# Kernel tuning notes

Measured on AMD Instinct MI355X. Metric: run time of the kernel, lower is better.

## Reference

```python
import jax, jax.numpy as jnp
import numpy as np

MIN_NORM = 1e-15
BALL_EPS = 4e-3  # fp32 boundary eps used by HGCN PoincareBall.proj
C = 1.0
RATIO = 0.75


def _norm(x):
    return jnp.clip(jnp.sqrt(jnp.sum(x * x, axis=-1, keepdims=True)), MIN_NORM)


def artanh(x):
    return jnp.arctanh(jnp.clip(x, -1.0 + 1e-7, 1.0 - 1e-7))


def proj(x, c):
    n = _norm(x)
    maxnorm = (1.0 - BALL_EPS) / jnp.sqrt(c)
    return jnp.where(n > maxnorm, x / n * maxnorm, x)


def expmap0(u, c):
    sc = jnp.sqrt(c)
    un = _norm(u)
    return jnp.tanh(sc * un) * u / (sc * un)


def logmap0(p, c):
    sc = jnp.sqrt(c)
    pn = _norm(p)
    return artanh(sc * pn) * p / (sc * pn)


def mobius_matvec(m, x, c):
    sc = jnp.sqrt(c)
    xn = _norm(x)
    mx = x @ m.T  # [N, out]
    mxn = _norm(mx)
    res = jnp.tanh(mxn / xn * artanh(sc * xn)) * mx / (mxn * sc)
    zero = jnp.all(mx == 0, axis=-1, keepdims=True)
    return jnp.where(zero, jnp.zeros_like(res), res)


def mobius_add(x, y, c):
    x2 = jnp.sum(x * x, axis=-1, keepdims=True)
    y2 = jnp.sum(y * y, axis=-1, keepdims=True)
    xy = jnp.sum(x * y, axis=-1, keepdims=True)
    num = (1 + 2 * c * xy + c * y2) * x + (1 - c * x2) * y
    den = 1 + 2 * c * xy + c * c * x2 * y2
    return num / jnp.maximum(den, MIN_NORM)


def hyp_linear(x, W, b, c):
    res = proj(mobius_matvec(W, x, c), c)
    hb = proj(expmap0(b[None, :], c), c)  # proj_tan0 is identity in Poincare ball
    return proj(mobius_add(res, hb, c), c)


def setup_inputs() -> dict:
    key = jax.random.key(0)
    k = jax.random.split(key, 6)
    N, E, D_IN, D_OUT = 50000, 800000, 128, 64
    x = 0.01 * jax.random.normal(k[0], (N, D_IN), jnp.float32)  # points near origin of ball
    W = jax.random.normal(k[1], (D_OUT, D_IN), jnp.float32) * np.sqrt(2.0 / (D_IN + D_OUT))
    b = 0.01 * jax.random.normal(k[2], (D_OUT,), jnp.float32)
    beta_W = jax.random.normal(k[3], (1, 2 * D_OUT), jnp.float32) * np.sqrt(2.0 / (2 * D_OUT + 1))
    beta_b = 0.01 * jax.random.normal(k[4], (1,), jnp.float32)
    edge_index = jax.random.randint(k[5], (2, E), 0, N, dtype=jnp.int64)
    return {"x": x, "W": W, "b": b, "beta_W": beta_W, "beta_b": beta_b, "edge_index": edge_index}


def reference(x, W, b, beta_W, beta_b, edge_index):
    N = x.shape[0]
    src, dst = edge_index[0], edge_index[1]  # PyG: x_j = x[src], aggregated at dst
    agg = lambda v: jax.ops.segment_sum(v[src], dst, num_segments=N)

    updated_x = hyp_linear(x, W, b, C)
    updated_tanx = logmap0(updated_x, C)

    # NodeInformationScore: (I - D^{-1/2} A D^{-1/2}) x, self loops removed (weight 0)
    w = jnp.where(src == dst, 0.0, 1.0).astype(x.dtype)
    deg = jax.ops.segment_sum(w, src, num_segments=N)
    dinv = jnp.where(deg > 0, deg ** -0.5, 0.0)
    norm_e = dinv[src] * w * dinv[dst]  # [E]
    neigh = jax.ops.segment_sum(norm_e[:, None] * updated_tanx[src], dst, num_segments=N)
    info = updated_tanx - neigh
    score = jnp.sum(jnp.abs(info), axis=1)  # [N]

    k = int(N * RATIO)
    T = jax.lax.top_k(score, k)[0][-1]  # min of top-k values
    sel = (score > T).astype(x.dtype)[:, None]  # [N, 1] hard gate

    sum_neigh = agg(updated_tanx)
    sum_sel = agg(sel * updated_tanx)
    concat = jnp.concatenate([sum_sel, sum_neigh], axis=-1)  # [N, 2*out]
    hyp_sums = proj(expmap0(concat, C), C)

    beta_out = hyp_linear(hyp_sums, beta_W, beta_b, C)  # [N, 1]
    w_sel = jax.nn.sigmoid(logmap0(beta_out, C))  # [N, 1]

    A_x = jax.nn.relu(agg(w_sel * sel * updated_tanx))
    out = proj(expmap0(updated_tanx + A_x, C), C)
    return out
```

## Files before the change

kernel.cpp:

```cpp
#include <hip/hip_runtime.h>
#include <math.h>
#include <limits.h>


__device__ __forceinline__ float wredsum(float v) {
#pragma unroll
    for (int off = 32; off > 0; off >>= 1) v += __shfl_xor(v, off, 64);
    return v;
}

__device__ __forceinline__ float rdlane_f(float v, int i) {
    return __uint_as_float(__builtin_amdgcn_readlane(__float_as_uint(v), i));
}

__device__ __forceinline__ int bitonic64(int val, int lane) {
#pragma unroll
    for (int k = 2; k <= 64; k <<= 1) {
#pragma unroll
        for (int j = k >> 1; j > 0; j >>= 1) {
            int other = __shfl_xor(val, j, 64);
            bool asc = ((lane & k) == 0);
            bool lower = ((lane & j) == 0);
            val = (asc == lower) ? min(val, other) : max(val, other);
        }
    }
    return val;
}

__device__ __forceinline__ float artanh_pos(float z) {
    z = fminf(z, 1.0f - 1e-7f);
    return 0.5f * (log1pf(z) - log1pf(-z));
}

__device__ __forceinline__ unsigned short f2bf(float f) {
    unsigned u = __float_as_uint(f);
    unsigned r = 0x7FFFu + ((u >> 16) & 1u);
    return (unsigned short)((u + r) >> 16);
}
__device__ __forceinline__ float bf2f(unsigned short h) {
    return __uint_as_float(((unsigned)h) << 16);
}

#define MAXNORM 0.996f
#define MINNORM 1e-15f
#define SLOT    64
#define GRP_CAP 5120


__global__ void k_transW(const float* __restrict__ W, float* __restrict__ WT) {
    int idx = blockIdx.x * 256 + threadIdx.x;
    if (idx >= 64 * 128) return;
    int o = idx >> 7, k = idx & 127;
    WT[k * 64 + o] = W[idx];
}


__global__ __launch_bounds__(256) void k_linear(
    const float* __restrict__ x, const float* __restrict__ WTg,
    const float* __restrict__ b, float* __restrict__ utx,
    unsigned short* __restrict__ utx16, int N)
{
    __shared__ float wt[8192];
    __shared__ float xq4[4][64];
    __shared__ float hb_s[64];
    int tid = threadIdx.x;
    int wave = tid >> 6, lane = tid & 63;
    int wave_u = __builtin_amdgcn_readfirstlane(wave);
    int r_hi = lane >> 3, o_hi = lane & 7;

    {
        const float4* src = (const float4*)WTg;
        float4* dst = (float4*)wt;
        for (int i = tid; i < 2048; i += 256) dst[i] = src[i];
    }
    if (wave == 0) {
        float bv = b[lane];
        float bn = fmaxf(sqrtf(wredsum(bv * bv)), MINNORM);
        float h = tanhf(bn) / bn * bv;
        float hn = fmaxf(sqrtf(wredsum(h * h)), MINNORM);
        if (hn > MAXNORM) h *= MAXNORM / hn;
        hb_s[lane] = h;
    }
    __syncthreads();

    int rbase = blockIdx.x * 64;
    const float4* xr4[8];
#pragma unroll
    for (int j = 0; j < 8; ++j)
        xr4[j] = (const float4*)(x + (size_t)min(rbase + r_hi * 8 + j, N - 1) * 128);

    float acc[64];
#pragma unroll
    for (int e = 0; e < 64; ++e) acc[e] = 0.f;
    float xsq8[8];
#pragma unroll
    for (int j = 0; j < 8; ++j) xsq8[j] = 0.f;

    int kb = wave_u * 32;
    for (int q = 0; q < 8; ++q) {
        int c = wave_u * 8 + q;
        float4 xq[8];
#pragma unroll
        for (int j = 0; j < 8; ++j)
            xq[j] = xr4[j][c];
        float wreg[4][8];
#pragma unroll
        for (int i = 0; i < 4; ++i) {
            float4 lo = *(const float4*)(wt + (kb + q * 4 + i) * 64 + o_hi * 8);
            float4 hi = *(const float4*)(wt + (kb + q * 4 + i) * 64 + o_hi * 8 + 4);
            wreg[i][0] = lo.x; wreg[i][1] = lo.y; wreg[i][2] = lo.z; wreg[i][3] = lo.w;
            wreg[i][4] = hi.x; wreg[i][5] = hi.y; wreg[i][6] = hi.z; wreg[i][7] = hi.w;
        }
#pragma unroll
        for (int j = 0; j < 8; ++j) {
#pragma unroll
            for (int oj = 0; oj < 8; ++oj) {
                acc[j * 8 + oj] += xq[j].x * wreg[0][oj] + xq[j].y * wreg[1][oj]
                                 + xq[j].z * wreg[2][oj] + xq[j].w * wreg[3][oj];
            }
            xsq8[j] += xq[j].x * xq[j].x + xq[j].y * xq[j].y
                     + xq[j].z * xq[j].z + xq[j].w * xq[j].w;
        }
    }

    if (o_hi == 0) {
#pragma unroll
        for (int j = 0; j < 8; ++j) xq4[wave_u][r_hi * 8 + j] = xsq8[j];
    }
    __syncthreads();

    float* redp = wt;
#pragma unroll
    for (int c = 0; c < 4; ++c) {
        if (wave_u != 0) {
#pragma unroll
            for (int r = 0; r < 16; ++r) redp[(wave_u - 1) * 1024 + r * 64 + lane] = acc[c * 16 + r];
        }
        __syncthreads();
        if (wave_u == 0) {
#pragma unroll
            for (int r = 0; r < 16; ++r)
                acc[c * 16 + r] += redp[0 * 1024 + r * 64 + lane]
                                 + redp[1 * 1024 + r * 64 + lane]
                                 + redp[2 * 1024 + r * 64 + lane];
        }
        __syncthreads();
    }

    float* eT = wt + 3072;
    if (wave_u == 0) {
#pragma unroll
        for (int j = 0; j < 8; ++j) {
            float4 v0 = { acc[j * 8 + 0], acc[j * 8 + 1], acc[j * 8 + 2], acc[j * 8 + 3] };
            float4 v1 = { acc[j * 8 + 4], acc[j * 8 + 5], acc[j * 8 + 6], acc[j * 8 + 7] };
            *(float4*)(eT + (r_hi * 8 + j) * 68 + o_hi * 8) = v0;
            *(float4*)(eT + (r_hi * 8 + j) * 68 + o_hi * 8 + 4) = v1;
        }
    }
    __syncthreads();
    if (wave_u != 0) return;

    float a2[64];
#pragma unroll
    for (int c4 = 0; c4 < 16; ++c4) {
        float4 v = *(const float4*)(eT + lane * 68 + c4 * 4);
        a2[c4 * 4 + 0] = v.x; a2[c4 * 4 + 1] = v.y;
        a2[c4 * 4 + 2] = v.z; a2[c4 * 4 + 3] = v.w;
    }
    float xsq = xq4[0][lane];
    xsq += xq4[1][lane] + xq4[2][lane] + xq4[3][lane];

    int row = blockIdx.x * 64 + lane;
    bool valid = row < N;

    float mx2 = 0.f;
#pragma unroll
    for (int o = 0; o < 64; ++o) mx2 += a2[o] * a2[o];

    float xn  = fmaxf(sqrtf(xsq), MINNORM);
    float mxn = fmaxf(sqrtf(mx2), MINNORM);
    float fac = tanhf(mxn / xn * artanh_pos(xn)) / mxn;
    float rn  = fac * mxn;
    if (rn > MAXNORM) { fac *= MAXNORM / rn; rn = MAXNORM; }
    float x2 = rn * rn;

    float hv_ = hb_s[lane];
    float hb2 = wredsum(hv_ * hv_);

    float xy = 0.f;
#pragma unroll
    for (int o = 0; o < 64; ++o) xy += (fac * a2[o]) * hb_s[o];

    float den = fmaxf(1.f + 2.f * xy + x2 * hb2, MINNORM);
    float ca  = (1.f + 2.f * xy + hb2) / den;
    float cb  = (1.f - x2) / den;

    float pn2 = 0.f;
#pragma unroll
    for (int o = 0; o < 64; ++o) {
        float p = ca * (fac * a2[o]) + cb * hb_s[o];
        a2[o] = p;
        pn2 += p * p;
    }
    float pn  = fmaxf(sqrtf(pn2), MINNORM);
    float psc = (pn > MAXNORM) ? (MAXNORM / pn) : 1.0f;
    float qn  = fmaxf(pn * psc, MINNORM);
    float lfac = artanh_pos(qn) / qn * psc;

    if (valid) {
        float* orow = utx + (size_t)row * 64;
        unsigned short* orow16 = utx16 + (size_t)row * 64;
#pragma unroll
        for (int o = 0; o < 64; o += 4) {
            float4 ov = { a2[o] * lfac, a2[o + 1] * lfac,
                          a2[o + 2] * lfac, a2[o + 3] * lfac };
            *(float4*)(orow + o) = ov;
            ushort4 hv = { f2bf(ov.x), f2bf(ov.y), f2bf(ov.z), f2bf(ov.w) };
            *(ushort4*)(orow16 + o) = hv;
        }
    }
}


__global__ __launch_bounds__(256) void k_partA(
    const int* __restrict__ ei, int E,
    int* cursD, int* cursS, unsigned* __restrict__ recD,
    unsigned char* __restrict__ recS)
{
    __shared__ int hD[256], hS[256], bD[256], bS[256];
    int tid = threadIdx.x;
    hD[tid] = 0; hS[tid] = 0;
    __syncthreads();
    int base = blockIdx.x * 4096;
    int sv[16], dv[16];
#pragma unroll
    for (int i = 0; i < 16; ++i) {
        int e = base + tid + i * 256;
        if (e < E) {
            sv[i] = ei[e]; dv[i] = ei[E + e];
            atomicAdd(&hD[dv[i] >> 8], 1);
            if (sv[i] != dv[i]) atomicAdd(&hS[sv[i] >> 8], 1);
        } else sv[i] = -1;
    }
    __syncthreads();
    if (hD[tid]) bD[tid] = atomicAdd(&cursD[tid], hD[tid]);
    if (hS[tid]) bS[tid] = atomicAdd(&cursS[tid], hS[tid]);
    __syncthreads();
    hD[tid] = 0; hS[tid] = 0;
    __syncthreads();
#pragma unroll
    for (int i = 0; i < 16; ++i) {
        if (sv[i] < 0) continue;
        int gD = dv[i] >> 8;
        int p = bD[gD] + atomicAdd(&hD[gD], 1);
        if (p < GRP_CAP)
            recD[(size_t)gD * GRP_CAP + p] = (unsigned)sv[i] | ((unsigned)(dv[i] & 255) << 16);
        if (sv[i] != dv[i]) {
            int gS = sv[i] >> 8;
            int q = bS[gS] + atomicAdd(&hS[gS], 1);
            if (q < GRP_CAP)
                recS[(size_t)gS * GRP_CAP + q] = (unsigned char)(sv[i] & 255);
        }
    }
}

__global__ __launch_bounds__(256) void k_Bfused(
    const int* __restrict__ cursD, const unsigned* __restrict__ recD,
    const int* __restrict__ cursS, const unsigned char* __restrict__ recS,
    int* __restrict__ cnt, int* __restrict__ slots, float* __restrict__ dinv, int N)
{
    __shared__ int lcnt[256];
    __shared__ int lslot[256 * SLOT];
    __shared__ unsigned hdeg[256];
    int g = blockIdx.x, tid = threadIdx.x;
    lcnt[tid] = 0; hdeg[tid] = 0;
    __syncthreads();
    int mS = min(cursS[g], GRP_CAP);
    const unsigned char* rS = recS + (size_t)g * GRP_CAP;
    for (int i = tid; i < mS; i += 256) atomicAdd(&hdeg[rS[i]], 1u);
    int m = min(cursD[g], GRP_CAP);
    const unsigned* r = recD + (size_t)g * GRP_CAP;
    for (int i = tid; i < m; i += 256) {
        unsigned v = r[i];
        int dlo = v >> 16, s = (int)(v & 0xFFFFu);
        int p = atomicAdd(&lcnt[dlo], 1);
        if (p < SLOT) lslot[dlo * SLOT + p] = s;
    }
    __syncthreads();
    int nbase = g * 256;
    if (nbase + tid < N) {
        cnt[nbase + tid] = lcnt[tid];
        unsigned dg = hdeg[tid];
        dinv[nbase + tid] = dg > 0 ? 1.0f / sqrtf((float)dg) : 0.0f;
    }
    int wave = tid >> 6, lane = tid & 63;
    for (int j = 0; j < 64; ++j) {
        int node = wave * 64 + j;
        if (nbase + node >= N) break;
        int d = min(lcnt[node], SLOT);
        if (lane < d)
            slots[(size_t)(nbase + node) * SLOT + lane] = lslot[node * SLOT + lane];
    }
}


__global__ __launch_bounds__(256) void k_pass1(
    const float* __restrict__ utx, const int* __restrict__ cnt,
    const int* __restrict__ slots, const float* __restrict__ dinv,
    float* __restrict__ score, float* __restrict__ sumn, int N)
{
    int wid = (blockIdx.x * 256 + threadIdx.x) >> 6;
    int lane = threadIdx.x & 63;
    if (wid >= N) return;
    int d = min(cnt[wid], SLOT);
    int val = (lane < d) ? slots[(size_t)wid * SLOT + lane] : INT_MAX;
    val = bitonic64(val, lane);
    int sval = (lane < d) ? val : wid;
    float dn = dinv[wid];
    float wv = (lane < d && sval != wid) ? dn * dinv[sval] : 0.f;
    float wn = (lane < d) ? 1.0f : 0.0f;

    float accn = 0.f, accs = 0.f;
    for (int i0 = 0; i0 < d; i0 += 8) {
#pragma unroll
        for (int j = 0; j < 8; ++j) {
            int i = i0 + j;
            int   s = __builtin_amdgcn_readlane(sval, i);
            float w = rdlane_f(wv, i);
            float n = rdlane_f(wn, i);
            float v = utx[(size_t)s * 64 + lane];
            accn += w * v;
            accs += n * v;
        }
    }
    float info = utx[(size_t)wid * 64 + lane] - accn;
    float sc = wredsum(fabsf(info));
    sumn[(size_t)wid * 64 + lane] = accs;
    if (lane == 0) score[wid] = sc;
}


__global__ __launch_bounds__(256) void k_hist8(
    const float* __restrict__ score, unsigned* __restrict__ hist,
    const unsigned* __restrict__ scal, int N, int pass)
{
    __shared__ unsigned lh[256];
    int tid = threadIdx.x;
    lh[tid] = 0;
    __syncthreads();
    int n = blockIdx.x * 256 + tid;
    if (n < N) {
        unsigned bits = __float_as_uint(score[n]);
        bool active = (pass == 0) || (((bits ^ scal[0]) >> (32 - 8 * pass)) == 0u);
        if (active) atomicAdd(&lh[(bits >> (24 - 8 * pass)) & 0xFFu], 1u);
    }
    __syncthreads();
    unsigned c = lh[tid];
    if (c) atomicAdd(&hist[tid], c);
}

__global__ __launch_bounds__(256) void k_pick8(
    const unsigned* __restrict__ hist, unsigned* scal, int K, int pass)
{
    __shared__ unsigned h[256];
    int t = threadIdx.x;
    h[t] = hist[t];
    __syncthreads();
    if (t == 0) {
        unsigned R = (pass == 0) ? (unsigned)K : scal[1];
        unsigned acc = 0;
        int B = 0;
        for (int bin = 255; bin >= 0; --bin) {
            if (acc + h[bin] >= R) { B = bin; break; }
            acc += h[bin];
        }
        unsigned prefix = (pass == 0) ? 0u : scal[0];
        scal[0] = prefix | ((unsigned)B << (24 - 8 * pass));
        scal[1] = R - acc;
        if (pass == 3) scal[2] = scal[0];
    }
}


__global__ __launch_bounds__(256) void k_sums_corr(
    const unsigned short* __restrict__ utx16, const int* __restrict__ cnt,
    const int* __restrict__ slots, const float* __restrict__ score,
    const unsigned* __restrict__ scal,
    const float* __restrict__ sumn, float* __restrict__ sums, int N)
{
    int wid = (blockIdx.x * 256 + threadIdx.x) >> 6;
    int lane = threadIdx.x & 63;
    if (wid >= N) return;
    float T = __uint_as_float(scal[2]);
    int d = min(cnt[wid], SLOT);
    int val = (lane < d) ? slots[(size_t)wid * SLOT + lane] : INT_MAX;
    val = bitonic64(val, lane);
    int sval = (lane < d) ? val : wid;
    float wc = (lane < d) ? ((score[sval] > T) ? 0.0f : 1.0f) : 0.0f;

    float corr = 0.f;
    for (int i0 = 0; i0 < d; i0 += 8) {
#pragma unroll
        for (int j = 0; j < 8; ++j) {
            int i = i0 + j;
            float w = rdlane_f(wc, i);
            int   s = __builtin_amdgcn_readlane(sval, i);
            if (w != 0.f)
                corr += bf2f(utx16[(size_t)s * 64 + lane]);
        }
    }
    size_t o = (size_t)wid * 64 + lane;
    sums[o] = sumn[o] - corr;
}


__global__ __launch_bounds__(256) void k_beta(
    const float* __restrict__ sumn, const float* __restrict__ sums,
    const float* __restrict__ beta_W, const float* __restrict__ beta_b,
    const float* __restrict__ score, const unsigned* __restrict__ scal,
    float* __restrict__ wsel, int N)
{
    int n = blockIdx.x * 256 + threadIdx.x;
    if (n >= N) return;
    const float4* su4 = (const float4*)(sums + (size_t)n * 64);
    const float4* sn4 = (const float4*)(sumn + (size_t)n * 64);
    float s_uu = 0.f, s_ub = 0.f;
#pragma unroll
    for (int k4 = 0; k4 < 16; ++k4) {
        float4 u0 = su4[k4];
        float4 u1 = sn4[k4];
        float4 b0 = *(const float4*)(beta_W + k4 * 4);
        float4 b1 = *(const float4*)(beta_W + 64 + k4 * 4);
        s_uu += u0.x * u0.x + u0.y * u0.y + u0.z * u0.z + u0.w * u0.w
              + u1.x * u1.x + u1.y * u1.y + u1.z * u1.z + u1.w * u1.w;
        s_ub += u0.x * b0.x + u0.y * b0.y + u0.z * b0.z + u0.w * b0.w
              + u1.x * b1.x + u1.y * b1.y + u1.z * b1.z + u1.w * b1.w;
    }
    float un = fmaxf(sqrtf(s_uu), MINNORM);
    float f  = tanhf(un) / un;
    float hn = fmaxf(f * un, MINNORM);
    float psc1 = (hn > MAXNORM) ? (MAXNORM / hn) : 1.0f;
    float xn = fmaxf(hn * psc1, MINNORM);
    float mx = f * psc1 * s_ub;
    float mxn = fmaxf(fabsf(mx), MINNORM);
    float res = tanhf(mxn / xn * artanh_pos(xn)) * mx / mxn;
    float rn = fmaxf(fabsf(res), MINNORM);
    if (rn > MAXNORM) res = res / rn * MAXNORM;
    float bb = beta_b[0];
    float bn = fmaxf(fabsf(bb), MINNORM);
    float hb = tanhf(bn) / bn * bb;
    float hbn = fmaxf(fabsf(hb), MINNORM);
    if (hbn > MAXNORM) hb = hb / hbn * MAXNORM;
    float x2 = res * res, y2 = hb * hb, xy = res * hb;
    float num = (1.f + 2.f * xy + y2) * res + (1.f - x2) * hb;
    float den = 1.f + 2.f * xy + x2 * y2;
    float p = num / fmaxf(den, MINNORM);
    float pn = fmaxf(fabsf(p), MINNORM);
    if (pn > MAXNORM) p = p / pn * MAXNORM;
    float qn = fmaxf(fabsf(p), MINNORM);
    float lg = artanh_pos(qn) * p / qn;
    float w = 1.f / (1.f + expf(-lg));
    float T = __uint_as_float(scal[2]);
    wsel[n] = (score[n] > T) ? w : 0.0f;
}


__global__ __launch_bounds__(256) void k_axout(
    const float* __restrict__ utx, const unsigned short* __restrict__ utx16,
    const int* __restrict__ cnt, const int* __restrict__ slots,
    const float* __restrict__ wsel, float* __restrict__ out, int N)
{
    int wid = (blockIdx.x * 256 + threadIdx.x) >> 6;
    int lane = threadIdx.x & 63;
    if (wid >= N) return;
    int d = min(cnt[wid], SLOT);
    int val = (lane < d) ? slots[(size_t)wid * SLOT + lane] : INT_MAX;
    val = bitonic64(val, lane);
    int sval = (lane < d) ? val : wid;
    float wa = (lane < d) ? wsel[sval] : 0.0f;

    float acc = 0.f;
    for (int i0 = 0; i0 < d; i0 += 8) {
#pragma unroll
        for (int j = 0; j < 8; ++j) {
            int i = i0 + j;
            int   s = __builtin_amdgcn_readlane(sval, i);
            float w = rdlane_f(wa, i);
            acc += w * bf2f(utx16[(size_t)s * 64 + lane]);
        }
    }
    float a = fmaxf(acc, 0.f);
    float u = utx[(size_t)wid * 64 + lane] + a;
    float un = fmaxf(sqrtf(wredsum(u * u)), MINNORM);
    float o = tanhf(un) / un * u;
    float on = fmaxf(sqrtf(wredsum(o * o)), MINNORM);
    if (on > MAXNORM) o *= MAXNORM / on;
    out[(size_t)wid * 64 + lane] = o;
}


extern "C" void kernel_launch(void* const* d_in, const int* in_sizes, int n_in,
                              void* d_out, int out_size, void* d_ws, size_t ws_size,
                              hipStream_t stream)
{
    const float* x      = (const float*)d_in[0];
    const float* W      = (const float*)d_in[1];
    const float* b      = (const float*)d_in[2];
    const float* beta_W = (const float*)d_in[3];
    const float* beta_b = (const float*)d_in[4];
    const int*   ei     = (const int*)d_in[5];

    const int N = in_sizes[0] / 128;
    const int E = in_sizes[5] / 2;
    const int K = (int)((double)N * 0.75);
    float* out = (float*)d_out;

    const int gG = (N + 255) / 256;

    char* ws = (char*)d_ws;
    size_t off = 0;
    auto alloc = [&](size_t bytes) -> void* {
        void* p = ws + off;
        off = (off + bytes + 255) & ~(size_t)255;
        return p;
    };
    float*          utx    = (float*)alloc((size_t)N * 64 * 4);
    unsigned short* utx16  = (unsigned short*)alloc((size_t)N * 64 * 2);
    float*          sumn   = (float*)alloc((size_t)N * 64 * 4);
    float*          sums   = (float*)alloc((size_t)N * 64 * 4);
    float*          score  = (float*)alloc((size_t)N * 4);
    float*          dinv   = (float*)alloc((size_t)N * 4);
    float*          wsel   = (float*)alloc((size_t)N * 4);
    int*            cnt    = (int*)alloc((size_t)N * 4);
    int*            slots  = (int*)alloc((size_t)N * SLOT * 4);
    float*          WT     = (float*)alloc(64 * 128 * 4);
    unsigned*       recD   = (unsigned*)alloc((size_t)gG * GRP_CAP * 4);
    unsigned char*  recS   = (unsigned char*)alloc((size_t)gG * GRP_CAP);
    unsigned*       scal   = (unsigned*)alloc(64);
    char*           zbase  = (char*)alloc(0);
    unsigned*       hist8  = (unsigned*)alloc(4 * 256 * 4);
    int*            cursD  = (int*)alloc(256 * 4);
    int*            cursS  = (int*)alloc(256 * 4);
    size_t          zbytes = (size_t)(((char*)(cursS + 256)) - zbase);
    if (off > ws_size) return;

    hipMemsetAsync(zbase, 0, zbytes, stream);

    int gN  = (N + 255) / 256;
    int gW  = (N + 3) / 4;
    int gLin = (N + 63) / 64;
    int gA  = (E + 4095) / 4096;

    k_transW<<<32, 256, 0, stream>>>(W, WT);
    k_linear<<<gLin, 256, 0, stream>>>(x, WT, b, utx, utx16, N);
    k_partA<<<gA, 256, 0, stream>>>(ei, E, cursD, cursS, recD, recS);
    k_Bfused<<<gG, 256, 0, stream>>>(cursD, recD, cursS, recS, cnt, slots, dinv, N);
    k_pass1<<<gW, 256, 0, stream>>>(utx, cnt, slots, dinv, score, sumn, N);
    for (int pass = 0; pass < 4; ++pass) {
        k_hist8<<<gN, 256, 0, stream>>>(score, hist8 + 256 * pass, scal, N, pass);
        k_pick8<<<1, 256, 0, stream>>>(hist8 + 256 * pass, scal, K, pass);
    }
    k_sums_corr<<<gW, 256, 0, stream>>>(utx16, cnt, slots, score, scal, sumn, sums, N);
    k_beta<<<gN, 256, 0, stream>>>(sumn, sums, beta_W, beta_b, score, scal, wsel, N);
    k_axout<<<gW, 256, 0, stream>>>(utx, utx16, cnt, slots, wsel, out, N);
}
```

Measured before the change: 251.9 us.

## Merge linear and edge-partition kernels; use 3-pass 11-bit radix select

The edge bucketing (partA) blocks are appended to the linear-layer kernel's grid so both independent stages run in a single launch and can overlap. The top-k threshold radix select changes from four 8-bit passes to three passes of 11/11/10 bits, which removes two kernel launches. The pick step uses a two-level scan over segment sums. In exchange, the merged kernel's shared memory footprint applies to the partition blocks too, and the larger histograms add more zeroing and flushing work.

After: 220.7 us (median of 2 runs). 1.14x faster.

```diff
diff --git a/kernel.cpp b/kernel.cpp
--- a/kernel.cpp
+++ b/kernel.cpp
@@ -55,15 +55,60 @@
 }
 
 
-__global__ __launch_bounds__(256) void k_linear(
+__global__ __launch_bounds__(256) void k_mega(
     const float* __restrict__ x, const float* __restrict__ WTg,
     const float* __restrict__ b, float* __restrict__ utx,
-    unsigned short* __restrict__ utx16, int N)
+    unsigned short* __restrict__ utx16, int N, int gLin,
+    const int* __restrict__ ei, int E,
+    int* cursD, int* cursS, unsigned* __restrict__ recD,
+    unsigned char* __restrict__ recS)
 {
     __shared__ float wt[8192];
     __shared__ float xq4[4][64];
     __shared__ float hb_s[64];
     int tid = threadIdx.x;
+
+    if ((int)blockIdx.x >= gLin) {
+        int* hD = (int*)wt;
+        int* hS = hD + 256;
+        int* bD = hS + 256;
+        int* bS = bD + 256;
+        hD[tid] = 0; hS[tid] = 0;
+        __syncthreads();
+        int base = ((int)blockIdx.x - gLin) * 4096;
+        int sv[16], dv[16];
+#pragma unroll
+        for (int i = 0; i < 16; ++i) {
+            int e = base + tid + i * 256;
+            if (e < E) {
+                sv[i] = ei[e]; dv[i] = ei[E + e];
+                atomicAdd(&hD[dv[i] >> 8], 1);
+                if (sv[i] != dv[i]) atomicAdd(&hS[sv[i] >> 8], 1);
+            } else sv[i] = -1;
+        }
+        __syncthreads();
+        if (hD[tid]) bD[tid] = atomicAdd(&cursD[tid], hD[tid]);
+        if (hS[tid]) bS[tid] = atomicAdd(&cursS[tid], hS[tid]);
+        __syncthreads();
+        hD[tid] = 0; hS[tid] = 0;
+        __syncthreads();
+#pragma unroll
+        for (int i = 0; i < 16; ++i) {
+            if (sv[i] < 0) continue;
+            int gD = dv[i] >> 8;
+            int p = bD[gD] + atomicAdd(&hD[gD], 1);
+            if (p < GRP_CAP)
+                recD[(size_t)gD * GRP_CAP + p] = (unsigned)sv[i] | ((unsigned)(dv[i] & 255) << 16);
+            if (sv[i] != dv[i]) {
+                int gS = sv[i] >> 8;
+                int q = bS[gS] + atomicAdd(&hS[gS], 1);
+                if (q < GRP_CAP)
+                    recS[(size_t)gS * GRP_CAP + q] = (unsigned char)(sv[i] & 255);
+            }
+        }
+        return;
+    }
+
     int wave = tid >> 6, lane = tid & 63;
     int wave_u = __builtin_amdgcn_readfirstlane(wave);
     int r_hi = lane >> 3, o_hi = lane & 7;
@@ -217,49 +262,6 @@
             *(float4*)(orow + o) = ov;
             ushort4 hv = { f2bf(ov.x), f2bf(ov.y), f2bf(ov.z), f2bf(ov.w) };
             *(ushort4*)(orow16 + o) = hv;
-        }
-    }
-}
-
-
-__global__ __launch_bounds__(256) void k_partA(
-    const int* __restrict__ ei, int E,
-    int* cursD, int* cursS, unsigned* __restrict__ recD,
-    unsigned char* __restrict__ recS)
-{
-    __shared__ int hD[256], hS[256], bD[256], bS[256];
-    int tid = threadIdx.x;
-    hD[tid] = 0; hS[tid] = 0;
-    __syncthreads();
-    int base = blockIdx.x * 4096;
-    int sv[16], dv[16];
-#pragma unroll
-    for (int i = 0; i < 16; ++i) {
-        int e = base + tid + i * 256;
-        if (e < E) {
-            sv[i] = ei[e]; dv[i] = ei[E + e];
-            atomicAdd(&hD[dv[i] >> 8], 1);
-            if (sv[i] != dv[i]) atomicAdd(&hS[sv[i] >> 8], 1);
-        } else sv[i] = -1;
-    }
-    __syncthreads();
-    if (hD[tid]) bD[tid] = atomicAdd(&cursD[tid], hD[tid]);
-    if (hS[tid]) bS[tid] = atomicAdd(&cursS[tid], hS[tid]);
-    __syncthreads();
-    hD[tid] = 0; hS[tid] = 0;
-    __syncthreads();
-#pragma unroll
-    for (int i = 0; i < 16; ++i) {
-        if (sv[i] < 0) continue;
-        int gD = dv[i] >> 8;
-        int p = bD[gD] + atomicAdd(&hD[gD], 1);
-        if (p < GRP_CAP)
-            recD[(size_t)gD * GRP_CAP + p] = (unsigned)sv[i] | ((unsigned)(dv[i] & 255) << 16);
-        if (sv[i] != dv[i]) {
-            int gS = sv[i] >> 8;
-            int q = bS[gS] + atomicAdd(&hS[gS], 1);
-            if (q < GRP_CAP)
-                recS[(size_t)gS * GRP_CAP + q] = (unsigned char)(sv[i] & 255);
         }
     }
 }
@@ -340,44 +342,65 @@
 }
 
 
-__global__ __launch_bounds__(256) void k_hist8(
+__global__ __launch_bounds__(256) void k_hist11(
     const float* __restrict__ score, unsigned* __restrict__ hist,
     const unsigned* __restrict__ scal, int N, int pass)
 {
-    __shared__ unsigned lh[256];
+    __shared__ unsigned lh[2048];
     int tid = threadIdx.x;
-    lh[tid] = 0;
+#pragma unroll
+    for (int i = 0; i < 8; ++i) lh[tid + i * 256] = 0;
     __syncthreads();
     int n = blockIdx.x * 256 + tid;
     if (n < N) {
         unsigned bits = __float_as_uint(score[n]);
-        bool active = (pass == 0) || (((bits ^ scal[0]) >> (32 - 8 * pass)) == 0u);
-        if (active) atomicAdd(&lh[(bits >> (24 - 8 * pass)) & 0xFFu], 1u);
-    }
-    __syncthreads();
-    unsigned c = lh[tid];
-    if (c) atomicAdd(&hist[tid], c);
-}
-
-__global__ __launch_bounds__(256) void k_pick8(
+        int bin; bool active;
+        if (pass == 0)      { active = true;                              bin = bits >> 21; }
+        else if (pass == 1) { active = ((bits ^ scal[0]) >> 21) == 0u;    bin = (bits >> 10) & 0x7FF; }
+        else                { active = ((bits ^ scal[0]) >> 10) == 0u;    bin = bits & 0x3FF; }
+        if (active) atomicAdd(&lh[bin], 1u);
+    }
+    __syncthreads();
+#pragma unroll
+    for (int i = 0; i < 8; ++i) {
+        unsigned c = lh[tid + i * 256];
+        if (c) atomicAdd(&hist[tid + i * 256], c);
+    }
+}
+
+__global__ __launch_bounds__(256) void k_pick11(
     const unsigned* __restrict__ hist, unsigned* scal, int K, int pass)
 {
-    __shared__ unsigned h[256];
+    __shared__ unsigned h[2048];
+    __shared__ unsigned seg[256];
     int t = threadIdx.x;
-    h[t] = hist[t];
+    unsigned s = 0;
+#pragma unroll
+    for (int i = 0; i < 8; ++i) {
+        unsigned v = hist[t * 8 + i];
+        h[t * 8 + i] = v;
+        s += v;
+    }
+    seg[t] = s;
     __syncthreads();
     if (t == 0) {
         unsigned R = (pass == 0) ? (unsigned)K : scal[1];
         unsigned acc = 0;
-        int B = 0;
-        for (int bin = 255; bin >= 0; --bin) {
-            if (acc + h[bin] >= R) { B = bin; break; }
-            acc += h[bin];
-        }
-        unsigned prefix = (pass == 0) ? 0u : scal[0];
-        scal[0] = prefix | ((unsigned)B << (24 - 8 * pass));
+        int S = 0;
+        for (int si = 255; si >= 0; --si) {
+            if (acc + seg[si] >= R) { S = si; break; }
+            acc += seg[si];
+        }
+        int B = S * 8;
+        for (int bin = S * 8 + 7; bin >= S * 8; --bin) {
+            unsigned hv = h[bin];
+            if (acc + hv >= R) { B = bin; break; }
+            acc += hv;
+        }
+        if (pass == 0)      { scal[0] = (unsigned)B << 21; }
+        else if (pass == 1) { scal[0] |= (unsigned)B << 10; }
+        else                { scal[2] = scal[0] | (unsigned)B; }
         scal[1] = R - acc;
-        if (pass == 3) scal[2] = scal[0];
     }
 }
 
@@ -538,7 +561,7 @@
     unsigned char*  recS   = (unsigned char*)alloc((size_t)gG * GRP_CAP);
     unsigned*       scal   = (unsigned*)alloc(64);
     char*           zbase  = (char*)alloc(0);
-    unsigned*       hist8  = (unsigned*)alloc(4 * 256 * 4);
+    unsigned*       hist11 = (unsigned*)alloc(3 * 2048 * 4);
     int*            cursD  = (int*)alloc(256 * 4);
     int*            cursS  = (int*)alloc(256 * 4);
     size_t          zbytes = (size_t)(((char*)(cursS + 256)) - zbase);
@@ -552,13 +575,13 @@
     int gA  = (E + 4095) / 4096;
 
     k_transW<<<32, 256, 0, stream>>>(W, WT);
-    k_linear<<<gLin, 256, 0, stream>>>(x, WT, b, utx, utx16, N);
-    k_partA<<<gA, 256, 0, stream>>>(ei, E, cursD, cursS, recD, recS);
+    k_mega<<<gLin + gA, 256, 0, stream>>>(x, WT, b, utx, utx16, N, gLin,
+                                          ei, E, cursD, cursS, recD, recS);
     k_Bfused<<<gG, 256, 0, stream>>>(cursD, recD, cursS, recS, cnt, slots, dinv, N);
     k_pass1<<<gW, 256, 0, stream>>>(utx, cnt, slots, dinv, score, sumn, N);
-    for (int pass = 0; pass < 4; ++pass) {
-        k_hist8<<<gN, 256, 0, stream>>>(score, hist8 + 256 * pass, scal, N, pass);
-        k_pick8<<<1, 256, 0, stream>>>(hist8 + 256 * pass, scal, K, pass);
+    for (int pass = 0; pass < 3; ++pass) {
+        k_hist11<<<gN, 256, 0, stream>>>(score, hist11 + 2048 * pass, scal, N, pass);
+        k_pick11<<<1, 256, 0, stream>>>(hist11 + 2048 * pass, scal, K, pass);
     }
     k_sums_corr<<<gW, 256, 0, stream>>>(utx16, cnt, slots, score, scal, sumn, sums, N);
     k_beta<<<gN, 256, 0, stream>>>(sumn, sums, beta_W, beta_b, score, scal, wsel, N);
```
